# Kernel tuning notes

Measured on AMD Instinct MI355X. Metric: run time of the kernel, lower is better.

## Reference

```python
import jax, jax.numpy as jnp
import numpy as np

C = 256          # hidden_channel
FFN = 1024       # ffn_channel
NCLS = 10
BS, N = 2, 2048  # batch, num_proposals
GRID = 180.0     # grid_size/out_size_factor
EPS_OT = 10.0
IPOT_ITERS = 100


def _ln(x, g, b, eps=1e-5):
    mu = jnp.mean(x, axis=-1, keepdims=True)
    var = jnp.var(x, axis=-1, keepdims=True)
    return (x - mu) * jax.lax.rsqrt(var + eps) * g + b


def setup_inputs() -> dict:
    key = jax.random.key(0)
    ks = jax.random.split(key, 32)
    s = 0.02
    inp = {
        "pts_query_feat": jax.random.normal(ks[0], (BS, C, N), jnp.float32),
        "pts_query_pos": jax.random.uniform(ks[1], (BS, N, 2), jnp.float32) * GRID,
        "img_query_feat": jax.random.normal(ks[2], (BS, C, N), jnp.float32),
        "img_query_pos": jax.random.uniform(ks[3], (BS, N, 2), jnp.float32) * GRID,
        "pts_cls": jax.random.normal(ks[4], (BS, NCLS, N), jnp.float32),
        "img_cls": jax.random.normal(ks[5], (BS, NCLS, N), jnp.float32),
        # pts/img 1x1-conv projections
        "Wp": jax.random.normal(ks[6], (C, C), jnp.float32) * s,
        "bp": jnp.zeros((C,), jnp.float32),
        "Wi": jax.random.normal(ks[7], (C, C), jnp.float32) * s,
        "bi": jnp.zeros((C,), jnp.float32),
        # learned position embeddings (2 -> C)
        "Wqp": jax.random.normal(ks[8], (C, 2), jnp.float32) * s,
        "bqp": jnp.zeros((C,), jnp.float32),
        "Wkp": jax.random.normal(ks[9], (C, 2), jnp.float32) * s,
        "bkp": jnp.zeros((C,), jnp.float32),
        # out_projection: Linear(2C, C) + LayerNorm(C)
        "Wout": jax.random.normal(ks[10], (C, 2 * C), jnp.float32) * s,
        "bout": jnp.zeros((C,), jnp.float32),
        "g_out": jnp.ones((C,), jnp.float32),
        "beta_out": jnp.zeros((C,), jnp.float32),
        # ffn
        "Wf1": jax.random.normal(ks[11], (FFN, C), jnp.float32) * s,
        "bf1": jnp.zeros((FFN,), jnp.float32),
        "Wf2": jax.random.normal(ks[12], (C, FFN), jnp.float32) * s,
        "bf2": jnp.zeros((C,), jnp.float32),
        # final LayerNorm
        "g_ln": jnp.ones((C,), jnp.float32),
        "b_ln": jnp.zeros((C,), jnp.float32),
        # prediction head: 1x1 conv C -> 2 (center)
        "Wpred": jax.random.normal(ks[13], (2, C), jnp.float32) * s,
        "bpred": jnp.zeros((2,), jnp.float32),
    }
    return inp


def ipot(pts_feat, img_feat, pts_cls, img_cls, cost):
    # pts_feat/img_feat: [bs, C, N]; pts_cls/img_cls: [bs, N]; cost: [bs, N, N]
    n = pts_cls.shape[1]
    b0 = jnp.ones_like(pts_cls) / n
    G = jnp.exp(-cost / EPS_OT)
    res0 = jnp.ones_like(G)

    def step(carry, _):
        b, res = carry
        Q = jnp.maximum(G * res, 1e-6)
        a = pts_cls / (jnp.einsum("bnm,bm->bn", Q, b) + 1e-6)
        b = img_cls / (jnp.einsum("bnm,bn->bm", Q, a) + 1e-6)
        # diag_embed(a) @ Q @ diag_embed(b) == a[:,:,None] * Q * b[:,None,:]
        res = a[:, :, None] * Q * b[:, None, :]
        return (b, res), None

    (b, res), _ = jax.lax.scan(step, (b0, res0), None, length=IPOT_ITERS)
    # F.normalize(res, dim=2, p=1); res is nonnegative
    res = res / jnp.maximum(jnp.sum(jnp.abs(res), axis=2, keepdims=True), 1e-12)
    img_att = jnp.einsum("bnm,bcm->bcn", res, img_feat)  # [bs, C, N]
    return jnp.concatenate([pts_feat, img_att], axis=1)   # [bs, 2C, N]


def reference(pts_query_feat, pts_query_pos, img_query_feat, img_query_pos,
              pts_cls, img_cls,
              Wp, bp, Wi, bi, Wqp, bqp, Wkp, bkp,
              Wout, bout, g_out, beta_out,
              Wf1, bf1, Wf2, bf2, g_ln, b_ln, Wpred, bpred):
    # channel projections (1x1 conv over N)
    pf = jnp.einsum("oc,bcn->bon", Wp, pts_query_feat) + bp[:, None]
    imf = jnp.einsum("oc,bcn->bon", Wi, img_query_feat) + bi[:, None]
    # learned positional embeddings: [bs,N,2] -> [bs,C,N]
    pf = pf + jnp.einsum("cd,bnd->bcn", Wqp, pts_query_pos) + bqp[:, None]
    imf = imf + jnp.einsum("cd,bnd->bcn", Wkp, img_query_pos) + bkp[:, None]
    # detached per-proposal confidences
    pcls = jax.lax.stop_gradient(jnp.max(jax.nn.sigmoid(pts_cls), axis=1))
    icls = jax.lax.stop_gradient(jnp.max(jax.nn.sigmoid(img_cls), axis=1))
    # pairwise L2 cost [bs, N, N]
    diff = pts_query_pos[:, :, None, :] - img_query_pos[:, None, :, :]
    cost = jnp.sqrt(jnp.sum(diff * diff, axis=-1))
    feat = ipot(pf, imf, pcls, icls, cost)            # [bs, 2C, N]
    x = jnp.swapaxes(feat, 1, 2)                      # [bs, N, 2C]
    x = _ln(x @ Wout.T + bout, g_out, beta_out)       # out_projection
    ffn = jax.nn.relu(x @ Wf1.T + bf1) @ Wf2.T + bf2  # ffn
    x = ffn + x                                       # ffn(x) + dropout(x), eval mode
    x = jnp.swapaxes(_ln(x, g_ln, b_ln), 1, 2)        # [bs, C, N]
    center = jnp.einsum("oc,bcn->bon", Wpred, x) + bpred[:, None]
    center = center + jnp.swapaxes(pts_query_pos, 1, 2)  # [bs, 2, N]
    new_pos = jnp.swapaxes(jax.lax.stop_gradient(center), 1, 2)  # [bs, N, 2]
    return (x, new_pos, center)
```

## Files before the change

### kernel.cpp

```cpp
#include <hip/hip_runtime.h>
#include <hip/hip_bf16.h>

#define N2   2048
#define CH   256
#define FFNC 1024

#define OFF_Q      0u
#define OFF_IMFT   8388608u
#define OFF_PF     9437184u
#define OFF_CPART  10485760u
#define OFF_PCLS   11534336u
#define OFF_ICLS   11538432u
#define OFF_BVEC   11542528u
#define OFF_AVEC   11546624u
#define OFF_WOUTT  11550720u
#define OFF_WF1T   11681792u
#define OFF_WF2T   11943936u

__device__ __forceinline__ void blockReduce2(float& x, float& y, float* sred) {
    #pragma unroll
    for (int off = 32; off; off >>= 1) {
        x += __shfl_xor(x, off);
        y += __shfl_xor(y, off);
    }
    const int wave = threadIdx.x >> 6, lane = threadIdx.x & 63;
    if (lane == 0) { sred[wave] = x; sred[4 + wave] = y; }
    __syncthreads();
    x = sred[0] + sred[1] + sred[2] + sred[3];
    y = sred[4] + sred[5] + sred[6] + sred[7];
    __syncthreads();
}

__global__ void __launch_bounds__(256) cls_max_k(
    const float* __restrict__ pc, const float* __restrict__ ic,
    float* __restrict__ pcls, float* __restrict__ icls) {
    const int g = blockIdx.x * 256 + threadIdx.x;
    const int b = g >> 11, n = g & 2047;
    float m1 = -1e30f, m2 = -1e30f;
    #pragma unroll
    for (int k = 0; k < 10; ++k) {
        const float v1 = pc[((size_t)b * 10 + k) * N2 + n];
        const float v2 = ic[((size_t)b * 10 + k) * N2 + n];
        m1 = fmaxf(m1, 1.f / (1.f + __expf(-v1)));
        m2 = fmaxf(m2, 1.f / (1.f + __expf(-v2)));
    }
    pcls[g] = m1; icls[g] = m2;
}

__global__ void __launch_bounds__(256) transpose_k(
    const float* __restrict__ in, float* __restrict__ out, int R, int C) {
    __shared__ float t[32][33];
    const int nct = C >> 5;
    const int bx = blockIdx.x % nct, by = blockIdx.x / nct;
    const int c0 = bx * 32, r0 = by * 32;
    const int tx = threadIdx.x & 31, ty = threadIdx.x >> 5;
    #pragma unroll
    for (int i = 0; i < 4; ++i) {
        const int r = ty + i * 8;
        t[r][tx] = in[(size_t)(r0 + r) * C + c0 + tx];
    }
    __syncthreads();
    #pragma unroll
    for (int i = 0; i < 4; ++i) {
        const int r = ty + i * 8;
        out[(size_t)(c0 + r) * R + r0 + tx] = t[tx][r];
    }
}

__global__ void __launch_bounds__(256) proj_rows(
    const float* __restrict__ F, const float* __restrict__ WT,
    const float* __restrict__ bias, const float* __restrict__ Wpos,
    const float* __restrict__ bpos, const float* __restrict__ pos,
    float* __restrict__ outb) {
    const int b = blockIdx.x >> 8;
    const int n0 = (blockIdx.x & 255) * 8;
    const int tid = threadIdx.x;
    __shared__ float s_x[8][256];
    for (int idx = tid; idx < 2048; idx += 256) {
        const int r = idx & 7, c = idx >> 3;
        s_x[r][c] = F[((size_t)b * CH + c) * N2 + n0 + r];
    }
    __syncthreads();
    float acc[8] = {0, 0, 0, 0, 0, 0, 0, 0};
    for (int c = 0; c < 256; ++c) {
        const float w = WT[(size_t)c * CH + tid];
        #pragma unroll
        for (int r = 0; r < 8; ++r) acc[r] += s_x[r][c] * w;
    }
    const float badd = bias[tid] + bpos[tid];
    const float w0 = Wpos[tid * 2 + 0], w1 = Wpos[tid * 2 + 1];
    #pragma unroll
    for (int r = 0; r < 8; ++r) {
        const int n = n0 + r;
        const float p0 = pos[((size_t)b * N2 + n) * 2 + 0];
        const float p1 = pos[((size_t)b * N2 + n) * 2 + 1];
        outb[((size_t)b * N2 + n) * CH + tid] = acc[r] + badd + w0 * p0 + w1 * p1;
    }
}


__device__ __forceinline__ void load_cols(const float* ipos, int batch, int tid,
                                          float* ixr, float* iyr) {
    const float4* ip4 = (const float4*)(ipos + (size_t)batch * (N2 * 2));
    const float4 A = ip4[tid * 2], B = ip4[tid * 2 + 1];
    const float4 Cc = ip4[512 + tid * 2], D = ip4[512 + tid * 2 + 1];
    ixr[0] = A.x; iyr[0] = A.y; ixr[1] = A.z; iyr[1] = A.w;
    ixr[2] = B.x; iyr[2] = B.y; ixr[3] = B.z; iyr[3] = B.w;
    ixr[4] = Cc.x; iyr[4] = Cc.y; ixr[5] = Cc.z; iyr[5] = Cc.w;
    ixr[6] = D.x; iyr[6] = D.y; ixr[7] = D.z; iyr[7] = D.w;
}

__global__ void __launch_bounds__(256) ipot_init_k(
    float* __restrict__ Q, const float* __restrict__ ppos, const float* __restrict__ ipos,
    const float* __restrict__ pcls, float* __restrict__ avec, float* __restrict__ cpart) {
    const int blk = blockIdx.x;
    const int batch = blk >> 8;
    const int p = blk & 255;
    const int r0 = p * 8;
    const int tid = threadIdx.x, wave = tid >> 6, lane = tid & 63;
    __shared__ float s_tot[4][8];

    float ixr[8], iyr[8];
    load_cols(ipos, batch, tid, ixr, iyr);
    float px[8], py[8], pcl8[8];
    #pragma unroll
    for (int j = 0; j < 8; ++j) {
        px[j] = ppos[((size_t)batch * N2 + r0 + j) * 2 + 0];
        py[j] = ppos[((size_t)batch * N2 + r0 + j) * 2 + 1];
        pcl8[j] = pcls[batch * N2 + r0 + j];
    }
    float* Qb = Q + (size_t)batch * N2 * N2;
    float cs[8] = {0, 0, 0, 0, 0, 0, 0, 0};

    #pragma unroll
    for (int h = 0; h < 2; ++h) {
        float qn[4][8];
        float rd[4];
        #pragma unroll
        for (int jj = 0; jj < 4; ++jj) {
            const int j = 4 * h + jj;
            rd[jj] = 0.f;
            #pragma unroll
            for (int k = 0; k < 8; ++k) {
                const float dx = px[j] - ixr[k], dy = py[j] - iyr[k];
                qn[jj][k] = fmaxf(__expf(-0.1f * sqrtf(dx * dx + dy * dy)), 1e-6f);
                rd[jj] += qn[jj][k];
            }
            float4* row4 = (float4*)(Qb + (size_t)(r0 + j) * N2);
            float4 lo, hi;
            lo.x = qn[jj][0]; lo.y = qn[jj][1]; lo.z = qn[jj][2]; lo.w = qn[jj][3];
            hi.x = qn[jj][4]; hi.y = qn[jj][5]; hi.z = qn[jj][6]; hi.w = qn[jj][7];
            row4[tid] = lo; row4[256 + tid] = hi;
        }
        #pragma unroll
        for (int off = 32; off; off >>= 1) {
            #pragma unroll
            for (int jj = 0; jj < 4; ++jj) rd[jj] += __shfl_xor(rd[jj], off);
        }
        if (lane == 0) {
            #pragma unroll
            for (int jj = 0; jj < 4; ++jj) s_tot[wave][4 * h + jj] = rd[jj];
        }
        __syncthreads();
        #pragma unroll
        for (int jj = 0; jj < 4; ++jj) {
            const int j = 4 * h + jj;
            const float tot = s_tot[0][j] + s_tot[1][j] + s_tot[2][j] + s_tot[3][j];
            const float a = pcl8[j] / (tot * (1.f / 2048.f) + 1e-6f);
            if (tid == 0) avec[batch * N2 + r0 + j] = a;
            #pragma unroll
            for (int k = 0; k < 8; ++k) cs[k] += a * qn[jj][k];
        }
    }
    float4* cp4 = (float4*)(cpart + ((size_t)batch * 256 + p) * N2);
    float4 l, h4;
    l.x = cs[0]; l.y = cs[1]; l.z = cs[2]; l.w = cs[3];
    h4.x = cs[4]; h4.y = cs[5]; h4.z = cs[6]; h4.w = cs[7];
    cp4[tid] = l; cp4[256 + tid] = h4;
}

__global__ void __launch_bounds__(256) ipot_red_k(
    const float* __restrict__ cpart, const float* __restrict__ icls,
    float* __restrict__ bvec) {
    const int b = blockIdx.x >> 5;
    const int c0 = (blockIdx.x & 31) * 64;
    const int tid = threadIdx.x;
    const int c = tid & 63, pg = tid >> 6;
    __shared__ float s_part[4][64];
    const float* cpb = cpart + (size_t)b * 256 * N2 + c0 + c;
    float s = 0.f;
    #pragma unroll 8
    for (int k = 0; k < 64; ++k) s += cpb[(size_t)(pg + 4 * k) * N2];
    s_part[pg][c] = s;
    __syncthreads();
    if (tid < 64) {
        const float tot = s_part[0][tid] + s_part[1][tid] + s_part[2][tid] + s_part[3][tid];
        bvec[b * N2 + c0 + tid] = icls[b * N2 + c0 + tid] / (tot + 1e-6f);
    }
}

__global__ void __launch_bounds__(256) ipot_ur_k(
    float* __restrict__ Q, const float* __restrict__ ppos, const float* __restrict__ ipos,
    const float* __restrict__ pcls, const float* __restrict__ bvec,
    float* __restrict__ avec, float* __restrict__ cpart) {
    const int blk = blockIdx.x;
    const int batch = blk >> 8;
    const int p = blk & 255;
    const int r0 = p * 8;
    const int tid = threadIdx.x, wave = tid >> 6, lane = tid & 63;
    __shared__ float s_tot[4][8];

    float ixr[8], iyr[8];
    load_cols(ipos, batch, tid, ixr, iyr);
    float bb[8];
    {
        const float4* bv4 = (const float4*)(bvec + (size_t)batch * N2);
        const float4 l = bv4[tid], h4 = bv4[256 + tid];
        bb[0] = l.x; bb[1] = l.y; bb[2] = l.z; bb[3] = l.w;
        bb[4] = h4.x; bb[5] = h4.y; bb[6] = h4.z; bb[7] = h4.w;
    }
    float px[8], py[8], pcl8[8], a_cur[8];
    #pragma unroll
    for (int j = 0; j < 8; ++j) {
        px[j] = ppos[((size_t)batch * N2 + r0 + j) * 2 + 0];
        py[j] = ppos[((size_t)batch * N2 + r0 + j) * 2 + 1];
        pcl8[j] = pcls[batch * N2 + r0 + j];
        a_cur[j] = avec[batch * N2 + r0 + j];
    }
    float* Qb = Q + (size_t)batch * N2 * N2;
    float cs[8] = {0, 0, 0, 0, 0, 0, 0, 0};

    #pragma unroll
    for (int h = 0; h < 2; ++h) {
        float qn[4][8];
        float rd[4];
        #pragma unroll
        for (int jj = 0; jj < 4; ++jj) {
            const int j = 4 * h + jj;
            float4* row4 = (float4*)(Qb + (size_t)(r0 + j) * N2);
            const float4 lo = row4[tid], hi = row4[256 + tid];
            float qv[8];
            qv[0] = lo.x; qv[1] = lo.y; qv[2] = lo.z; qv[3] = lo.w;
            qv[4] = hi.x; qv[5] = hi.y; qv[6] = hi.z; qv[7] = hi.w;
            rd[jj] = 0.f;
            const float a = a_cur[j];
            #pragma unroll
            for (int k = 0; k < 8; ++k) {
                const float dx = px[j] - ixr[k], dy = py[j] - iyr[k];
                const float G = __expf(-0.1f * sqrtf(dx * dx + dy * dy));
                const float v = fmaxf(G * ((a * qv[k]) * bb[k]), 1e-6f);
                qn[jj][k] = v;
                rd[jj] += v * bb[k];
            }
            float4 lo2, hi2;
            lo2.x = qn[jj][0]; lo2.y = qn[jj][1]; lo2.z = qn[jj][2]; lo2.w = qn[jj][3];
            hi2.x = qn[jj][4]; hi2.y = qn[jj][5]; hi2.z = qn[jj][6]; hi2.w = qn[jj][7];
            row4[tid] = lo2; row4[256 + tid] = hi2;
        }
        #pragma unroll
        for (int off = 32; off; off >>= 1) {
            #pragma unroll
            for (int jj = 0; jj < 4; ++jj) rd[jj] += __shfl_xor(rd[jj], off);
        }
        if (lane == 0) {
            #pragma unroll
            for (int jj = 0; jj < 4; ++jj) s_tot[wave][4 * h + jj] = rd[jj];
        }
        __syncthreads();
        #pragma unroll
        for (int jj = 0; jj < 4; ++jj) {
            const int j = 4 * h + jj;
            const float tot = s_tot[0][j] + s_tot[1][j] + s_tot[2][j] + s_tot[3][j];
            const float a = pcl8[j] / (tot + 1e-6f);
            if (tid == 0) avec[batch * N2 + r0 + j] = a;
            #pragma unroll
            for (int k = 0; k < 8; ++k) cs[k] += a * qn[jj][k];
        }
    }
    float4* cp4 = (float4*)(cpart + ((size_t)batch * 256 + p) * N2);
    float4 l, h4;
    l.x = cs[0]; l.y = cs[1]; l.z = cs[2]; l.w = cs[3];
    h4.x = cs[4]; h4.y = cs[5]; h4.z = cs[6]; h4.w = cs[7];
    cp4[tid] = l; cp4[256 + tid] = h4;
}

__global__ void __launch_bounds__(256) ipot_fin_k(
    float* __restrict__ Q, const float* __restrict__ pcls,
    const float* __restrict__ bvec, const float* __restrict__ avec) {
    const int blk = blockIdx.x;
    const int batch = blk >> 8;
    const int p = blk & 255;
    const int r0 = p * 8;
    const int tid = threadIdx.x, wave = tid >> 6, lane = tid & 63;
    __shared__ float s_tot[4][8];

    float bb[8];
    {
        const float4* bv4 = (const float4*)(bvec + (size_t)batch * N2);
        const float4 l = bv4[tid], h4 = bv4[256 + tid];
        bb[0] = l.x; bb[1] = l.y; bb[2] = l.z; bb[3] = l.w;
        bb[4] = h4.x; bb[5] = h4.y; bb[6] = h4.z; bb[7] = h4.w;
    }
    float a8[8];
    #pragma unroll
    for (int j = 0; j < 8; ++j) a8[j] = avec[batch * N2 + r0 + j];
    float* Qb = Q + (size_t)batch * N2 * N2;

    #pragma unroll
    for (int h = 0; h < 2; ++h) {
        float vv[4][8];
        float rs[4];
        #pragma unroll
        for (int jj = 0; jj < 4; ++jj) {
            const int j = 4 * h + jj;
            float4* row4 = (float4*)(Qb + (size_t)(r0 + j) * N2);
            const float4 lo = row4[tid], hi = row4[256 + tid];
            float qv[8];
            qv[0] = lo.x; qv[1] = lo.y; qv[2] = lo.z; qv[3] = lo.w;
            qv[4] = hi.x; qv[5] = hi.y; qv[6] = hi.z; qv[7] = hi.w;
            rs[jj] = 0.f;
            const float a = a8[j];
            #pragma unroll
            for (int k = 0; k < 8; ++k) {
                const float v = (a * qv[k]) * bb[k];
                vv[jj][k] = v;
                rs[jj] += v;
            }
        }
        #pragma unroll
        for (int off = 32; off; off >>= 1) {
            #pragma unroll
            for (int jj = 0; jj < 4; ++jj) rs[jj] += __shfl_xor(rs[jj], off);
        }
        if (lane == 0) {
            #pragma unroll
            for (int jj = 0; jj < 4; ++jj) s_tot[wave][4 * h + jj] = rs[jj];
        }
        __syncthreads();
        #pragma unroll
        for (int jj = 0; jj < 4; ++jj) {
            const int j = 4 * h + jj;
            const float tot = s_tot[0][j] + s_tot[1][j] + s_tot[2][j] + s_tot[3][j];
            const float sc = 1.f / fmaxf(tot, 1e-12f);
            float4* row4 = (float4*)(Qb + (size_t)(r0 + j) * N2);
            float4 lo, hi;
            lo.x = vv[jj][0] * sc; lo.y = vv[jj][1] * sc;
            lo.z = vv[jj][2] * sc; lo.w = vv[jj][3] * sc;
            hi.x = vv[jj][4] * sc; hi.y = vv[jj][5] * sc;
            hi.z = vv[jj][6] * sc; hi.w = vv[jj][7] * sc;
            row4[tid] = lo; row4[256 + tid] = hi;
        }
    }
}

__global__ void __launch_bounds__(256) att_gemm(
    const float* __restrict__ R, const float* __restrict__ V, float* __restrict__ att) {
    const int bid = blockIdx.x;
    const int nt = bid & 31, ct = (bid >> 5) & 3, b = bid >> 7;
    const int n0 = nt * 64, c0 = ct * 64;
    __shared__ float sR[64][17];
    __shared__ float sV[16][65];
    const int tid = threadIdx.x;
    const int cx = tid & 15, ny = tid >> 4;
    float acc[4][4] = {};
    const float* Rb = R + (size_t)b * N2 * N2;
    const float* Vb = V + (size_t)b * N2 * CH;
    for (int k0 = 0; k0 < N2; k0 += 16) {
        for (int idx = tid; idx < 1024; idx += 256) {
            const int nl = idx >> 4, kk = idx & 15;
            sR[nl][kk] = Rb[(size_t)(n0 + nl) * N2 + k0 + kk];
        }
        for (int idx = tid; idx < 1024; idx += 256) {
            const int kk = idx >> 6, cl = idx & 63;
            sV[kk][cl] = Vb[(size_t)(k0 + kk) * CH + c0 + cl];
        }
        __syncthreads();
        #pragma unroll
        for (int kk = 0; kk < 16; ++kk) {
            float av[4], bv[4];
            #pragma unroll
            for (int i = 0; i < 4; ++i) av[i] = sR[ny + 16 * i][kk];
            #pragma unroll
            for (int j = 0; j < 4; ++j) bv[j] = sV[kk][cx + 16 * j];
            #pragma unroll
            for (int i = 0; i < 4; ++i)
                #pragma unroll
                for (int j = 0; j < 4; ++j) acc[i][j] += av[i] * bv[j];
        }
        __syncthreads();
    }
    #pragma unroll
    for (int i = 0; i < 4; ++i)
        #pragma unroll
        for (int j = 0; j < 4; ++j)
            att[((size_t)b * N2 + n0 + ny + 16 * i) * CH + c0 + cx + 16 * j] = acc[i][j];
}

__global__ void __launch_bounds__(256) outproj_k(
    const float* __restrict__ pf, const float* __restrict__ att,
    const float* __restrict__ WoutT,
    const float* __restrict__ bout, const float* __restrict__ g,
    const float* __restrict__ be, float* __restrict__ y) {
    const int b = blockIdx.x >> 8;
    const int n0 = (blockIdx.x & 255) * 8;
    const int tid = threadIdx.x;
    __shared__ float s_x[8][512];
    __shared__ float sred[8];
    for (int idx = tid; idx < 2048; idx += 256) {
        const int k = idx & 255, r = idx >> 8;
        s_x[r][k] = pf[((size_t)b * N2 + n0 + r) * CH + k];
        s_x[r][256 + k] = att[((size_t)b * N2 + n0 + r) * CH + k];
    }
    __syncthreads();
    float acc[8] = {0, 0, 0, 0, 0, 0, 0, 0};
    for (int k = 0; k < 512; ++k) {
        const float w = WoutT[(size_t)k * CH + tid];
        #pragma unroll
        for (int r = 0; r < 8; ++r) acc[r] += s_x[r][k] * w;
    }
    const float bo = bout[tid], gg = g[tid], bb = be[tid];
    #pragma unroll
    for (int r = 0; r < 8; ++r) {
        const float v = acc[r] + bo;
        float s1 = v, s2 = v * v;
        blockReduce2(s1, s2, sred);
        const float mu = s1 * (1.f / 256.f);
        const float var = s2 * (1.f / 256.f) - mu * mu;
        y[((size_t)b * N2 + n0 + r) * CH + tid] = (v - mu) * rsqrtf(var + 1e-5f) * gg + bb;
    }
}

__global__ void __launch_bounds__(256) ffn_k(
    const float* __restrict__ y, const float* __restrict__ Wf1T,
    const float* __restrict__ bf1, const float* __restrict__ Wf2T,
    const float* __restrict__ bf2, const float* __restrict__ gln,
    const float* __restrict__ bln, const float* __restrict__ Wpred,
    const float* __restrict__ bpred, const float* __restrict__ pos,
    float* __restrict__ y2, float* __restrict__ out1,
    float* __restrict__ out2) {
    const int b = blockIdx.x >> 8;
    const int n0 = (blockIdx.x & 255) * 8;
    const int tid = threadIdx.x;
    __shared__ float s_y[8][256];
    __shared__ float s_h[8][1024];
    __shared__ float sred[8];
    for (int idx = tid; idx < 2048; idx += 256) {
        const int c = idx & 255, r = idx >> 8;
        s_y[r][c] = y[((size_t)b * N2 + n0 + r) * CH + c];
    }
    __syncthreads();
    float acc[4][8] = {};
    for (int c = 0; c < 256; ++c) {
        float yv[8];
        #pragma unroll
        for (int r = 0; r < 8; ++r) yv[r] = s_y[r][c];
        #pragma unroll
        for (int fi = 0; fi < 4; ++fi) {
            const float w = Wf1T[(size_t)c * FFNC + fi * 256 + tid];
            #pragma unroll
            for (int r = 0; r < 8; ++r) acc[fi][r] += yv[r] * w;
        }
    }
    #pragma unroll
    for (int fi = 0; fi < 4; ++fi) {
        const int f = fi * 256 + tid;
        const float bb = bf1[f];
        #pragma unroll
        for (int r = 0; r < 8; ++r) s_h[r][f] = fmaxf(acc[fi][r] + bb, 0.f);
    }
    __syncthreads();
    float a2[8] = {0, 0, 0, 0, 0, 0, 0, 0};
    for (int f = 0; f < 1024; ++f) {
        const float w = Wf2T[(size_t)f * CH + tid];
        #pragma unroll
        for (int r = 0; r < 8; ++r) a2[r] += s_h[r][f] * w;
    }
    const float bfv = bf2[tid], gg = gln[tid], bb2 = bln[tid];
    const float wp0 = Wpred[tid], wp1 = Wpred[CH + tid];
    #pragma unroll
    for (int r = 0; r < 8; ++r) {
        const int n = n0 + r;
        const float v = a2[r] + bfv + s_y[r][tid];
        float s1 = v, s2 = v * v;
        blockReduce2(s1, s2, sred);
        const float mu = s1 * (1.f / 256.f);
        const float var = s2 * (1.f / 256.f) - mu * mu;
        const float xo = (v - mu) * rsqrtf(var + 1e-5f) * gg + bb2;
        y2[((size_t)b * N2 + n) * CH + tid] = xo;
        float d0 = wp0 * xo, d1 = wp1 * xo;
        blockReduce2(d0, d1, sred);
        if (tid == 0) {
            const float c0v = d0 + bpred[0] + pos[((size_t)b * N2 + n) * 2 + 0];
            const float c1v = d1 + bpred[1] + pos[((size_t)b * N2 + n) * 2 + 1];
            out2[((size_t)b * 2 + 0) * N2 + n] = c0v;
            out2[((size_t)b * 2 + 1) * N2 + n] = c1v;
            out1[((size_t)b * N2 + n) * 2 + 0] = c0v;
            out1[((size_t)b * N2 + n) * 2 + 1] = c1v;
        }
    }
}

__global__ void __launch_bounds__(256) out_x_k(
    const float* __restrict__ y2, float* __restrict__ out0) {
    __shared__ float t[32][33];
    const int bid = blockIdx.x;
    const int ct = bid & 7, nt = (bid >> 3) & 63, b = bid >> 9;
    const int tx = threadIdx.x & 31, ty = threadIdx.x >> 5;
    #pragma unroll
    for (int i = 0; i < 4; ++i) {
        const int r = ty + i * 8;
        t[r][tx] = y2[((size_t)b * N2 + nt * 32 + r) * CH + ct * 32 + tx];
    }
    __syncthreads();
    #pragma unroll
    for (int i = 0; i < 4; ++i) {
        const int r = ty + i * 8;
        out0[((size_t)b * CH + ct * 32 + r) * N2 + nt * 32 + tx] = t[tx][r];
    }
}

extern "C" void kernel_launch(void* const* d_in, const int* in_sizes, int n_in,
                              void* d_out, int out_size, void* d_ws, size_t ws_size,
                              hipStream_t stream) {
    const float* ptsf  = (const float*)d_in[0];
    const float* ppos  = (const float*)d_in[1];
    const float* imgf  = (const float*)d_in[2];
    const float* ipos  = (const float*)d_in[3];
    const float* pcin  = (const float*)d_in[4];
    const float* icin  = (const float*)d_in[5];
    const float* Wp    = (const float*)d_in[6];
    const float* bp    = (const float*)d_in[7];
    const float* Wi    = (const float*)d_in[8];
    const float* bi    = (const float*)d_in[9];
    const float* Wqp   = (const float*)d_in[10];
    const float* bqp   = (const float*)d_in[11];
    const float* Wkp   = (const float*)d_in[12];
    const float* bkp   = (const float*)d_in[13];
    const float* Wout  = (const float*)d_in[14];
    const float* bout  = (const float*)d_in[15];
    const float* gout  = (const float*)d_in[16];
    const float* beo   = (const float*)d_in[17];
    const float* Wf1   = (const float*)d_in[18];
    const float* bf1   = (const float*)d_in[19];
    const float* Wf2   = (const float*)d_in[20];
    const float* bf2   = (const float*)d_in[21];
    const float* gln   = (const float*)d_in[22];
    const float* bln   = (const float*)d_in[23];
    const float* Wpred = (const float*)d_in[24];
    const float* bpred = (const float*)d_in[25];

    float* ws    = (float*)d_ws;
    float* Q     = ws + OFF_Q;
    float* imfT  = ws + OFF_IMFT;
    float* pf    = ws + OFF_PF;
    float* cpart = ws + OFF_CPART;
    float* att   = ws + OFF_CPART;
    float* WpT   = ws + OFF_CPART;
    float* WiT   = ws + OFF_CPART + 65536u;
    float* pcls  = ws + OFF_PCLS;
    float* icls  = ws + OFF_ICLS;
    float* bvec  = ws + OFF_BVEC;
    float* avec  = ws + OFF_AVEC;
    float* WoutT = ws + OFF_WOUTT;
    float* Wf1T  = ws + OFF_WF1T;
    float* Wf2T  = ws + OFF_WF2T;
    float* yb    = ws + OFF_Q;
    float* y2    = ws + OFF_PF;

    float* out0 = (float*)d_out;
    float* out1 = out0 + (size_t)2 * CH * N2;
    float* out2 = out1 + (size_t)2 * N2 * 2;

    cls_max_k<<<16, 256, 0, stream>>>(pcin, icin, pcls, icls);
    transpose_k<<<64, 256, 0, stream>>>(Wp, WpT, 256, 256);
    transpose_k<<<64, 256, 0, stream>>>(Wi, WiT, 256, 256);
    transpose_k<<<128, 256, 0, stream>>>(Wout, WoutT, 256, 512);
    transpose_k<<<256, 256, 0, stream>>>(Wf1, Wf1T, 1024, 256);
    transpose_k<<<256, 256, 0, stream>>>(Wf2, Wf2T, 256, 1024);
    proj_rows<<<512, 256, 0, stream>>>(ptsf, WpT, bp, Wqp, bqp, ppos, pf);
    proj_rows<<<512, 256, 0, stream>>>(imgf, WiT, bi, Wkp, bkp, ipos, imfT);

    ipot_init_k<<<512, 256, 0, stream>>>(Q, ppos, ipos, pcls, avec, cpart);
    for (int t = 1; t < 100; ++t) {
        ipot_red_k<<<64, 256, 0, stream>>>(cpart, icls, bvec);
        ipot_ur_k<<<512, 256, 0, stream>>>(Q, ppos, ipos, pcls, bvec, avec, cpart);
    }
    ipot_red_k<<<64, 256, 0, stream>>>(cpart, icls, bvec);
    ipot_fin_k<<<512, 256, 0, stream>>>(Q, pcls, bvec, avec);

    att_gemm<<<256, 256, 0, stream>>>(Q, imfT, att);
    outproj_k<<<512, 256, 0, stream>>>(pf, att, WoutT, bout, gout, beo, yb);
    ffn_k<<<512, 256, 0, stream>>>(yb, Wf1T, bf1, Wf2T, bf2, gln, bln,
                                   Wpred, bpred, ppos, y2, out1, out2);
    out_x_k<<<1024, 256, 0, stream>>>(y2, out0);
}
```

Measured before the change: 2.645 ms.

## Halve IPOT rows per block, split-K attention GEMM with atomics, remap workspace

The IPOT init, update and finalize kernels now handle 4 rows per block instead of 8, which doubles the grid to 1024 blocks. It also doubles the column-partial buffer that the reduction kernel sums over. The attention GEMM is split four ways along K with atomicAdd accumulation into a zeroed buffer, and uses a transposed shared tile with float4 reads. The workspace is remapped so pf/yb/y2 reuse the Q region after IPOT, which moves the pts projection after the GEMM. The goal is more parallelism and occupancy for the 100 memory-bound iterations, at the cost of twice the cpart traffic in each reduction and atomic contention.

```diff
diff --git a/kernel.cpp b/kernel.cpp
--- a/kernel.cpp
+++ b/kernel.cpp
@@ -7,8 +7,7 @@
 
 #define OFF_Q      0u
 #define OFF_IMFT   8388608u
-#define OFF_PF     9437184u
-#define OFF_CPART  10485760u
+#define OFF_CPART  9437184u
 #define OFF_PCLS   11534336u
 #define OFF_ICLS   11538432u
 #define OFF_BVEC   11542528u
@@ -110,69 +109,64 @@
     ixr[6] = D.x; iyr[6] = D.y; ixr[7] = D.z; iyr[7] = D.w;
 }
 
-__global__ void __launch_bounds__(256) ipot_init_k(
+__global__ void __launch_bounds__(256, 4) ipot_init_k(
     float* __restrict__ Q, const float* __restrict__ ppos, const float* __restrict__ ipos,
     const float* __restrict__ pcls, float* __restrict__ avec, float* __restrict__ cpart) {
     const int blk = blockIdx.x;
-    const int batch = blk >> 8;
-    const int p = blk & 255;
-    const int r0 = p * 8;
+    const int batch = blk >> 9;
+    const int p = blk & 511;
+    const int r0 = p * 4;
     const int tid = threadIdx.x, wave = tid >> 6, lane = tid & 63;
-    __shared__ float s_tot[4][8];
+    __shared__ float s_tot[4][4];
 
     float ixr[8], iyr[8];
     load_cols(ipos, batch, tid, ixr, iyr);
-    float px[8], py[8], pcl8[8];
-    #pragma unroll
-    for (int j = 0; j < 8; ++j) {
+    float px[4], py[4], pcl4[4];
+    #pragma unroll
+    for (int j = 0; j < 4; ++j) {
         px[j] = ppos[((size_t)batch * N2 + r0 + j) * 2 + 0];
         py[j] = ppos[((size_t)batch * N2 + r0 + j) * 2 + 1];
-        pcl8[j] = pcls[batch * N2 + r0 + j];
+        pcl4[j] = pcls[batch * N2 + r0 + j];
     }
     float* Qb = Q + (size_t)batch * N2 * N2;
     float cs[8] = {0, 0, 0, 0, 0, 0, 0, 0};
 
-    #pragma unroll
-    for (int h = 0; h < 2; ++h) {
-        float qn[4][8];
-        float rd[4];
-        #pragma unroll
-        for (int jj = 0; jj < 4; ++jj) {
-            const int j = 4 * h + jj;
-            rd[jj] = 0.f;
-            #pragma unroll
-            for (int k = 0; k < 8; ++k) {
-                const float dx = px[j] - ixr[k], dy = py[j] - iyr[k];
-                qn[jj][k] = fmaxf(__expf(-0.1f * sqrtf(dx * dx + dy * dy)), 1e-6f);
-                rd[jj] += qn[jj][k];
-            }
-            float4* row4 = (float4*)(Qb + (size_t)(r0 + j) * N2);
-            float4 lo, hi;
-            lo.x = qn[jj][0]; lo.y = qn[jj][1]; lo.z = qn[jj][2]; lo.w = qn[jj][3];
-            hi.x = qn[jj][4]; hi.y = qn[jj][5]; hi.z = qn[jj][6]; hi.w = qn[jj][7];
-            row4[tid] = lo; row4[256 + tid] = hi;
-        }
-        #pragma unroll
-        for (int off = 32; off; off >>= 1) {
-            #pragma unroll
-            for (int jj = 0; jj < 4; ++jj) rd[jj] += __shfl_xor(rd[jj], off);
-        }
-        if (lane == 0) {
-            #pragma unroll
-            for (int jj = 0; jj < 4; ++jj) s_tot[wave][4 * h + jj] = rd[jj];
-        }
-        __syncthreads();
-        #pragma unroll
-        for (int jj = 0; jj < 4; ++jj) {
-            const int j = 4 * h + jj;
-            const float tot = s_tot[0][j] + s_tot[1][j] + s_tot[2][j] + s_tot[3][j];
-            const float a = pcl8[j] / (tot * (1.f / 2048.f) + 1e-6f);
-            if (tid == 0) avec[batch * N2 + r0 + j] = a;
-            #pragma unroll
-            for (int k = 0; k < 8; ++k) cs[k] += a * qn[jj][k];
-        }
-    }
-    float4* cp4 = (float4*)(cpart + ((size_t)batch * 256 + p) * N2);
+    float qn[4][8];
+    float rd[4];
+    #pragma unroll
+    for (int jj = 0; jj < 4; ++jj) {
+        rd[jj] = 0.f;
+        #pragma unroll
+        for (int k = 0; k < 8; ++k) {
+            const float dx = px[jj] - ixr[k], dy = py[jj] - iyr[k];
+            qn[jj][k] = fmaxf(__expf(-0.1f * sqrtf(dx * dx + dy * dy)), 1e-6f);
+            rd[jj] += qn[jj][k];
+        }
+        float4* row4 = (float4*)(Qb + (size_t)(r0 + jj) * N2);
+        float4 lo, hi;
+        lo.x = qn[jj][0]; lo.y = qn[jj][1]; lo.z = qn[jj][2]; lo.w = qn[jj][3];
+        hi.x = qn[jj][4]; hi.y = qn[jj][5]; hi.z = qn[jj][6]; hi.w = qn[jj][7];
+        row4[tid] = lo; row4[256 + tid] = hi;
+    }
+    #pragma unroll
+    for (int off = 32; off; off >>= 1) {
+        #pragma unroll
+        for (int jj = 0; jj < 4; ++jj) rd[jj] += __shfl_xor(rd[jj], off);
+    }
+    if (lane == 0) {
+        #pragma unroll
+        for (int jj = 0; jj < 4; ++jj) s_tot[wave][jj] = rd[jj];
+    }
+    __syncthreads();
+    #pragma unroll
+    for (int jj = 0; jj < 4; ++jj) {
+        const float tot = s_tot[0][jj] + s_tot[1][jj] + s_tot[2][jj] + s_tot[3][jj];
+        const float a = pcl4[jj] / (tot * (1.f / 2048.f) + 1e-6f);
+        if (tid == 0) avec[batch * N2 + r0 + jj] = a;
+        #pragma unroll
+        for (int k = 0; k < 8; ++k) cs[k] += a * qn[jj][k];
+    }
+    float4* cp4 = (float4*)(cpart + ((size_t)batch * 512 + p) * N2);
     float4 l, h4;
     l.x = cs[0]; l.y = cs[1]; l.z = cs[2]; l.w = cs[3];
     h4.x = cs[4]; h4.y = cs[5]; h4.z = cs[6]; h4.w = cs[7];
@@ -187,10 +181,10 @@
     const int tid = threadIdx.x;
     const int c = tid & 63, pg = tid >> 6;
     __shared__ float s_part[4][64];
-    const float* cpb = cpart + (size_t)b * 256 * N2 + c0 + c;
+    const float* cpb = cpart + (size_t)b * 512 * N2 + c0 + c;
     float s = 0.f;
     #pragma unroll 8
-    for (int k = 0; k < 64; ++k) s += cpb[(size_t)(pg + 4 * k) * N2];
+    for (int k = 0; k < 128; ++k) s += cpb[(size_t)(pg + 4 * k) * N2];
     s_part[pg][c] = s;
     __syncthreads();
     if (tid < 64) {
@@ -199,16 +193,16 @@
     }
 }
 
-__global__ void __launch_bounds__(256) ipot_ur_k(
+__global__ void __launch_bounds__(256, 4) ipot_ur_k(
     float* __restrict__ Q, const float* __restrict__ ppos, const float* __restrict__ ipos,
     const float* __restrict__ pcls, const float* __restrict__ bvec,
     float* __restrict__ avec, float* __restrict__ cpart) {
     const int blk = blockIdx.x;
-    const int batch = blk >> 8;
-    const int p = blk & 255;
-    const int r0 = p * 8;
+    const int batch = blk >> 9;
+    const int p = blk & 511;
+    const int r0 = p * 4;
     const int tid = threadIdx.x, wave = tid >> 6, lane = tid & 63;
-    __shared__ float s_tot[4][8];
+    __shared__ float s_tot[4][4];
 
     float ixr[8], iyr[8];
     load_cols(ipos, batch, tid, ixr, iyr);
@@ -219,80 +213,75 @@
         bb[0] = l.x; bb[1] = l.y; bb[2] = l.z; bb[3] = l.w;
         bb[4] = h4.x; bb[5] = h4.y; bb[6] = h4.z; bb[7] = h4.w;
     }
-    float px[8], py[8], pcl8[8], a_cur[8];
-    #pragma unroll
-    for (int j = 0; j < 8; ++j) {
+    float px[4], py[4], pcl4[4], a_cur[4];
+    #pragma unroll
+    for (int j = 0; j < 4; ++j) {
         px[j] = ppos[((size_t)batch * N2 + r0 + j) * 2 + 0];
         py[j] = ppos[((size_t)batch * N2 + r0 + j) * 2 + 1];
-        pcl8[j] = pcls[batch * N2 + r0 + j];
+        pcl4[j] = pcls[batch * N2 + r0 + j];
         a_cur[j] = avec[batch * N2 + r0 + j];
     }
     float* Qb = Q + (size_t)batch * N2 * N2;
     float cs[8] = {0, 0, 0, 0, 0, 0, 0, 0};
 
-    #pragma unroll
-    for (int h = 0; h < 2; ++h) {
-        float qn[4][8];
-        float rd[4];
-        #pragma unroll
-        for (int jj = 0; jj < 4; ++jj) {
-            const int j = 4 * h + jj;
-            float4* row4 = (float4*)(Qb + (size_t)(r0 + j) * N2);
-            const float4 lo = row4[tid], hi = row4[256 + tid];
-            float qv[8];
-            qv[0] = lo.x; qv[1] = lo.y; qv[2] = lo.z; qv[3] = lo.w;
-            qv[4] = hi.x; qv[5] = hi.y; qv[6] = hi.z; qv[7] = hi.w;
-            rd[jj] = 0.f;
-            const float a = a_cur[j];
-            #pragma unroll
-            for (int k = 0; k < 8; ++k) {
-                const float dx = px[j] - ixr[k], dy = py[j] - iyr[k];
-                const float G = __expf(-0.1f * sqrtf(dx * dx + dy * dy));
-                const float v = fmaxf(G * ((a * qv[k]) * bb[k]), 1e-6f);
-                qn[jj][k] = v;
-                rd[jj] += v * bb[k];
-            }
-            float4 lo2, hi2;
-            lo2.x = qn[jj][0]; lo2.y = qn[jj][1]; lo2.z = qn[jj][2]; lo2.w = qn[jj][3];
-            hi2.x = qn[jj][4]; hi2.y = qn[jj][5]; hi2.z = qn[jj][6]; hi2.w = qn[jj][7];
-            row4[tid] = lo2; row4[256 + tid] = hi2;
-        }
-        #pragma unroll
-        for (int off = 32; off; off >>= 1) {
-            #pragma unroll
-            for (int jj = 0; jj < 4; ++jj) rd[jj] += __shfl_xor(rd[jj], off);
-        }
-        if (lane == 0) {
-            #pragma unroll
-            for (int jj = 0; jj < 4; ++jj) s_tot[wave][4 * h + jj] = rd[jj];
-        }
-        __syncthreads();
-        #pragma unroll
-        for (int jj = 0; jj < 4; ++jj) {
-            const int j = 4 * h + jj;
-            const float tot = s_tot[0][j] + s_tot[1][j] + s_tot[2][j] + s_tot[3][j];
-            const float a = pcl8[j] / (tot + 1e-6f);
-            if (tid == 0) avec[batch * N2 + r0 + j] = a;
-            #pragma unroll
-            for (int k = 0; k < 8; ++k) cs[k] += a * qn[jj][k];
-        }
-    }
-    float4* cp4 = (float4*)(cpart + ((size_t)batch * 256 + p) * N2);
+    float qn[4][8];
+    float rd[4];
+    #pragma unroll
+    for (int jj = 0; jj < 4; ++jj) {
+        float4* row4 = (float4*)(Qb + (size_t)(r0 + jj) * N2);
+        const float4 lo = row4[tid], hi = row4[256 + tid];
+        float qv[8];
+        qv[0] = lo.x; qv[1] = lo.y; qv[2] = lo.z; qv[3] = lo.w;
+        qv[4] = hi.x; qv[5] = hi.y; qv[6] = hi.z; qv[7] = hi.w;
+        rd[jj] = 0.f;
+        const float a = a_cur[jj];
+        #pragma unroll
+        for (int k = 0; k < 8; ++k) {
+            const float dx = px[jj] - ixr[k], dy = py[jj] - iyr[k];
+            const float G = __expf(-0.1f * sqrtf(dx * dx + dy * dy));
+            const float v = fmaxf(G * ((a * qv[k]) * bb[k]), 1e-6f);
+            qn[jj][k] = v;
+            rd[jj] += v * bb[k];
+        }
+        float4 lo2, hi2;
+        lo2.x = qn[jj][0]; lo2.y = qn[jj][1]; lo2.z = qn[jj][2]; lo2.w = qn[jj][3];
+        hi2.x = qn[jj][4]; hi2.y = qn[jj][5]; hi2.z = qn[jj][6]; hi2.w = qn[jj][7];
+        row4[tid] = lo2; row4[256 + tid] = hi2;
+    }
+    #pragma unroll
+    for (int off = 32; off; off >>= 1) {
+        #pragma unroll
+        for (int jj = 0; jj < 4; ++jj) rd[jj] += __shfl_xor(rd[jj], off);
+    }
+    if (lane == 0) {
+        #pragma unroll
+        for (int jj = 0; jj < 4; ++jj) s_tot[wave][jj] = rd[jj];
+    }
+    __syncthreads();
+    #pragma unroll
+    for (int jj = 0; jj < 4; ++jj) {
+        const float tot = s_tot[0][jj] + s_tot[1][jj] + s_tot[2][jj] + s_tot[3][jj];
+        const float a = pcl4[jj] / (tot + 1e-6f);
+        if (tid == 0) avec[batch * N2 + r0 + jj] = a;
+        #pragma unroll
+        for (int k = 0; k < 8; ++k) cs[k] += a * qn[jj][k];
+    }
+    float4* cp4 = (float4*)(cpart + ((size_t)batch * 512 + p) * N2);
     float4 l, h4;
     l.x = cs[0]; l.y = cs[1]; l.z = cs[2]; l.w = cs[3];
     h4.x = cs[4]; h4.y = cs[5]; h4.z = cs[6]; h4.w = cs[7];
     cp4[tid] = l; cp4[256 + tid] = h4;
 }
 
-__global__ void __launch_bounds__(256) ipot_fin_k(
+__global__ void __launch_bounds__(256, 4) ipot_fin_k(
     float* __restrict__ Q, const float* __restrict__ pcls,
     const float* __restrict__ bvec, const float* __restrict__ avec) {
     const int blk = blockIdx.x;
-    const int batch = blk >> 8;
-    const int p = blk & 255;
-    const int r0 = p * 8;
+    const int batch = blk >> 9;
+    const int p = blk & 511;
+    const int r0 = p * 4;
     const int tid = threadIdx.x, wave = tid >> 6, lane = tid & 63;
-    __shared__ float s_tot[4][8];
+    __shared__ float s_tot[4][4];
 
     float bb[8];
     {
@@ -301,74 +290,75 @@
         bb[0] = l.x; bb[1] = l.y; bb[2] = l.z; bb[3] = l.w;
         bb[4] = h4.x; bb[5] = h4.y; bb[6] = h4.z; bb[7] = h4.w;
     }
-    float a8[8];
-    #pragma unroll
-    for (int j = 0; j < 8; ++j) a8[j] = avec[batch * N2 + r0 + j];
+    float a4[4];
+    #pragma unroll
+    for (int j = 0; j < 4; ++j) a4[j] = avec[batch * N2 + r0 + j];
     float* Qb = Q + (size_t)batch * N2 * N2;
 
-    #pragma unroll
-    for (int h = 0; h < 2; ++h) {
-        float vv[4][8];
-        float rs[4];
-        #pragma unroll
-        for (int jj = 0; jj < 4; ++jj) {
-            const int j = 4 * h + jj;
-            float4* row4 = (float4*)(Qb + (size_t)(r0 + j) * N2);
-            const float4 lo = row4[tid], hi = row4[256 + tid];
-            float qv[8];
-            qv[0] = lo.x; qv[1] = lo.y; qv[2] = lo.z; qv[3] = lo.w;
-            qv[4] = hi.x; qv[5] = hi.y; qv[6] = hi.z; qv[7] = hi.w;
-            rs[jj] = 0.f;
-            const float a = a8[j];
-            #pragma unroll
-            for (int k = 0; k < 8; ++k) {
-                const float v = (a * qv[k]) * bb[k];
-                vv[jj][k] = v;
-                rs[jj] += v;
-            }
-        }
-        #pragma unroll
-        for (int off = 32; off; off >>= 1) {
-            #pragma unroll
-            for (int jj = 0; jj < 4; ++jj) rs[jj] += __shfl_xor(rs[jj], off);
-        }
-        if (lane == 0) {
-            #pragma unroll
-            for (int jj = 0; jj < 4; ++jj) s_tot[wave][4 * h + jj] = rs[jj];
-        }
-        __syncthreads();
-        #pragma unroll
-        for (int jj = 0; jj < 4; ++jj) {
-            const int j = 4 * h + jj;
-            const float tot = s_tot[0][j] + s_tot[1][j] + s_tot[2][j] + s_tot[3][j];
-            const float sc = 1.f / fmaxf(tot, 1e-12f);
-            float4* row4 = (float4*)(Qb + (size_t)(r0 + j) * N2);
-            float4 lo, hi;
-            lo.x = vv[jj][0] * sc; lo.y = vv[jj][1] * sc;
-            lo.z = vv[jj][2] * sc; lo.w = vv[jj][3] * sc;
-            hi.x = vv[jj][4] * sc; hi.y = vv[jj][5] * sc;
-            hi.z = vv[jj][6] * sc; hi.w = vv[jj][7] * sc;
-            row4[tid] = lo; row4[256 + tid] = hi;
-        }
-    }
-}
-
-__global__ void __launch_bounds__(256) att_gemm(
+    float vv[4][8];
+    float rs[4];
+    #pragma unroll
+    for (int jj = 0; jj < 4; ++jj) {
+        float4* row4 = (float4*)(Qb + (size_t)(r0 + jj) * N2);
+        const float4 lo = row4[tid], hi = row4[256 + tid];
+        float qv[8];
+        qv[0] = lo.x; qv[1] = lo.y; qv[2] = lo.z; qv[3] = lo.w;
+        qv[4] = hi.x; qv[5] = hi.y; qv[6] = hi.z; qv[7] = hi.w;
+        rs[jj] = 0.f;
+        const float a = a4[jj];
+        #pragma unroll
+        for (int k = 0; k < 8; ++k) {
+            const float v = (a * qv[k]) * bb[k];
+            vv[jj][k] = v;
+            rs[jj] += v;
+        }
+    }
+    #pragma unroll
+    for (int off = 32; off; off >>= 1) {
+        #pragma unroll
+        for (int jj = 0; jj < 4; ++jj) rs[jj] += __shfl_xor(rs[jj], off);
+    }
+    if (lane == 0) {
+        #pragma unroll
+        for (int jj = 0; jj < 4; ++jj) s_tot[wave][jj] = rs[jj];
+    }
+    __syncthreads();
+    #pragma unroll
+    for (int jj = 0; jj < 4; ++jj) {
+        const float tot = s_tot[0][jj] + s_tot[1][jj] + s_tot[2][jj] + s_tot[3][jj];
+        const float sc = 1.f / fmaxf(tot, 1e-12f);
+        float4* row4 = (float4*)(Qb + (size_t)(r0 + jj) * N2);
+        float4 lo, hi;
+        lo.x = vv[jj][0] * sc; lo.y = vv[jj][1] * sc;
+        lo.z = vv[jj][2] * sc; lo.w = vv[jj][3] * sc;
+        hi.x = vv[jj][4] * sc; hi.y = vv[jj][5] * sc;
+        hi.z = vv[jj][6] * sc; hi.w = vv[jj][7] * sc;
+        row4[tid] = lo; row4[256 + tid] = hi;
+    }
+}
+
+__global__ void __launch_bounds__(256) att_zero_k(float* __restrict__ att) {
+    const int idx = blockIdx.x * 256 + threadIdx.x;
+    float4 z; z.x = 0.f; z.y = 0.f; z.z = 0.f; z.w = 0.f;
+    ((float4*)att)[idx] = z;
+}
+
+__global__ void __launch_bounds__(256, 4) att_gemm(
     const float* __restrict__ R, const float* __restrict__ V, float* __restrict__ att) {
     const int bid = blockIdx.x;
-    const int nt = bid & 31, ct = (bid >> 5) & 3, b = bid >> 7;
-    const int n0 = nt * 64, c0 = ct * 64;
-    __shared__ float sR[64][17];
-    __shared__ float sV[16][65];
+    const int nt = bid & 31, ct = (bid >> 5) & 3, ks = (bid >> 7) & 3, b = bid >> 9;
+    const int n0 = nt * 64, c0 = ct * 64, k00 = ks * 512;
+    __shared__ float sRT[16][68];
+    __shared__ float sV[16][68];
     const int tid = threadIdx.x;
-    const int cx = tid & 15, ny = tid >> 4;
+    const int ny = tid & 15, cx = tid >> 4;
     float acc[4][4] = {};
     const float* Rb = R + (size_t)b * N2 * N2;
     const float* Vb = V + (size_t)b * N2 * CH;
-    for (int k0 = 0; k0 < N2; k0 += 16) {
+    for (int k0 = k00; k0 < k00 + 512; k0 += 16) {
         for (int idx = tid; idx < 1024; idx += 256) {
             const int nl = idx >> 4, kk = idx & 15;
-            sR[nl][kk] = Rb[(size_t)(n0 + nl) * N2 + k0 + kk];
+            sRT[kk][nl] = Rb[(size_t)(n0 + nl) * N2 + k0 + kk];
         }
         for (int idx = tid; idx < 1024; idx += 256) {
             const int kk = idx >> 6, cl = idx & 63;
@@ -377,15 +367,12 @@
         __syncthreads();
         #pragma unroll
         for (int kk = 0; kk < 16; ++kk) {
-            float av[4], bv[4];
-            #pragma unroll
-            for (int i = 0; i < 4; ++i) av[i] = sR[ny + 16 * i][kk];
-            #pragma unroll
-            for (int j = 0; j < 4; ++j) bv[j] = sV[kk][cx + 16 * j];
-            #pragma unroll
-            for (int i = 0; i < 4; ++i)
-                #pragma unroll
-                for (int j = 0; j < 4; ++j) acc[i][j] += av[i] * bv[j];
+            const float4 av = *(const float4*)&sRT[kk][4 * ny];
+            const float4 bv = *(const float4*)&sV[kk][4 * cx];
+            acc[0][0] += av.x * bv.x; acc[0][1] += av.x * bv.y; acc[0][2] += av.x * bv.z; acc[0][3] += av.x * bv.w;
+            acc[1][0] += av.y * bv.x; acc[1][1] += av.y * bv.y; acc[1][2] += av.y * bv.z; acc[1][3] += av.y * bv.w;
+            acc[2][0] += av.z * bv.x; acc[2][1] += av.z * bv.y; acc[2][2] += av.z * bv.z; acc[2][3] += av.z * bv.w;
+            acc[3][0] += av.w * bv.x; acc[3][1] += av.w * bv.y; acc[3][2] += av.w * bv.z; acc[3][3] += av.w * bv.w;
         }
         __syncthreads();
     }
@@ -393,7 +380,7 @@
     for (int i = 0; i < 4; ++i)
         #pragma unroll
         for (int j = 0; j < 4; ++j)
-            att[((size_t)b * N2 + n0 + ny + 16 * i) * CH + c0 + cx + 16 * j] = acc[i][j];
+            atomicAdd(&att[((size_t)b * N2 + n0 + 4 * ny + i) * CH + c0 + 4 * cx + j], acc[i][j]);
 }
 
 __global__ void __launch_bounds__(256) outproj_k(
@@ -552,11 +539,9 @@
     float* ws    = (float*)d_ws;
     float* Q     = ws + OFF_Q;
     float* imfT  = ws + OFF_IMFT;
-    float* pf    = ws + OFF_PF;
     float* cpart = ws + OFF_CPART;
     float* att   = ws + OFF_CPART;
-    float* WpT   = ws + OFF_CPART;
-    float* WiT   = ws + OFF_CPART + 65536u;
+    float* WiT   = ws + OFF_CPART;
     float* pcls  = ws + OFF_PCLS;
     float* icls  = ws + OFF_ICLS;
     float* bvec  = ws + OFF_BVEC;
@@ -564,31 +549,35 @@
     float* WoutT = ws + OFF_WOUTT;
     float* Wf1T  = ws + OFF_WF1T;
     float* Wf2T  = ws + OFF_WF2T;
-    float* yb    = ws + OFF_Q;
-    float* y2    = ws + OFF_PF;
+    float* pf    = ws + OFF_Q;
+    float* yb    = ws + OFF_Q + 1048576u;
+    float* y2    = ws + OFF_Q + 2097152u;
+    float* WpT   = ws + OFF_Q + 3145728u;
 
     float* out0 = (float*)d_out;
     float* out1 = out0 + (size_t)2 * CH * N2;
     float* out2 = out1 + (size_t)2 * N2 * 2;
 
     cls_max_k<<<16, 256, 0, stream>>>(pcin, icin, pcls, icls);
-    transpose_k<<<64, 256, 0, stream>>>(Wp, WpT, 256, 256);
     transpose_k<<<64, 256, 0, stream>>>(Wi, WiT, 256, 256);
+    proj_rows<<<512, 256, 0, stream>>>(imgf, WiT, bi, Wkp, bkp, ipos, imfT);
     transpose_k<<<128, 256, 0, stream>>>(Wout, WoutT, 256, 512);
     transpose_k<<<256, 256, 0, stream>>>(Wf1, Wf1T, 1024, 256);
     transpose_k<<<256, 256, 0, stream>>>(Wf2, Wf2T, 256, 1024);
-    proj_rows<<<512, 256, 0, stream>>>(ptsf, WpT, bp, Wqp, bqp, ppos, pf);
-    proj_rows<<<512, 256, 0, stream>>>(imgf, WiT, bi, Wkp, bkp, ipos, imfT);
-
-    ipot_init_k<<<512, 256, 0, stream>>>(Q, ppos, ipos, pcls, avec, cpart);
+
+    ipot_init_k<<<1024, 256, 0, stream>>>(Q, ppos, ipos, pcls, avec, cpart);
     for (int t = 1; t < 100; ++t) {
         ipot_red_k<<<64, 256, 0, stream>>>(cpart, icls, bvec);
-        ipot_ur_k<<<512, 256, 0, stream>>>(Q, ppos, ipos, pcls, bvec, avec, cpart);
+        ipot_ur_k<<<1024, 256, 0, stream>>>(Q, ppos, ipos, pcls, bvec, avec, cpart);
     }
     ipot_red_k<<<64, 256, 0, stream>>>(cpart, icls, bvec);
-    ipot_fin_k<<<512, 256, 0, stream>>>(Q, pcls, bvec, avec);
-
-    att_gemm<<<256, 256, 0, stream>>>(Q, imfT, att);
+    ipot_fin_k<<<1024, 256, 0, stream>>>(Q, pcls, bvec, avec);
+
+    att_zero_k<<<1024, 256, 0, stream>>>(att);
+    att_gemm<<<1024, 256, 0, stream>>>(Q, imfT, att);
+
+    transpose_k<<<64, 256, 0, stream>>>(Wp, WpT, 256, 256);
+    proj_rows<<<512, 256, 0, stream>>>(ptsf, WpT, bp, Wqp, bqp, ppos, pf);
     outproj_k<<<512, 256, 0, stream>>>(pf, att, WoutT, bout, gout, beo, yb);
     ffn_k<<<512, 256, 0, stream>>>(yb, Wf1T, bf1, Wf2T, bf2, gln, bln,
                                    Wpred, bpred, ppos, y2, out1, out2);
```

Result: no change. 2.608 ms (-1.4%).
